# Kernel tuning notes

Hardware: AMD Instinct MI355X
Metric: run time of the kernel (lower is better)

Reference implementation:

```python
import jax, jax.numpy as jnp
import numpy as np

B, N, F = 4, 4096, 32
NG = 14  # number of gate graph-convs in GCNLSTM_Cell with memory state


def setup_inputs() -> dict:
    key = jax.random.key(0)
    ks = jax.random.split(key, 7)
    x = jax.random.normal(ks[0], (B, N, F), jnp.float32)
    h = jax.random.normal(ks[1], (B, N, F), jnp.float32)
    c = jax.random.normal(ks[2], (B, N, F), jnp.float32)
    m = jax.random.normal(ks[3], (B, N, F), jnp.float32)
    # weighted dense adjacency, scaled so row sums are O(1)
    adj = jax.random.uniform(ks[4], (N, N), jnp.float32) / N
    # 14 WeightedGraphConv layers: Dense F -> 2F (single FeedForward layer, no relu)
    W = jax.random.normal(ks[5], (NG, F, 2 * F), jnp.float32) * (1.0 / np.sqrt(F))
    b = jnp.zeros((NG, 2 * F), jnp.float32)
    return {"x": x, "h": h, "c": c, "m": m, "adj": adj, "W": W, "b": b}


def _gcn(ax, W, b):
    # ax: [B,N,F] = adj @ state (precomputed); Dense to 2F then GLU split.
    z = ax @ W + b  # [B,N,2F]
    ls, rs = jnp.split(z, 2, axis=-1)
    return ls * jax.nn.sigmoid(rs)


def reference(x, h, c, m, adj, W, b):
    # shared graph aggregation for x and h (adj is the same for all gates)
    ax = jnp.einsum('nm,bmf->bnf', adj, x)  # [B,N,F]
    ah = jnp.einsum('nm,bmf->bnf', adj, h)

    fx = _gcn(ax, W[0], b[0]); fh = _gcn(ah, W[1], b[1])
    ix = _gcn(ax, W[2], b[2]); ih = _gcn(ah, W[3], b[3])
    cx = _gcn(ax, W[4], b[4]); ch = _gcn(ah, W[5], b[5])
    ox = _gcn(ax, W[6], b[6]); oh = _gcn(ah, W[7], b[7])

    f = jax.nn.sigmoid(fx + fh)
    i = jax.nn.sigmoid(ix + ih)
    o = jax.nn.sigmoid(ox + oh)
    c_new = f * c + i * jnp.tanh(cx + ch)
    h1 = o * jnp.tanh(c_new)

    # memory-state block (6 more graph convs on h1 and m)
    ah1 = jnp.einsum('nm,bmf->bnf', adj, h1)
    am = jnp.einsum('nm,bmf->bnf', adj, m)
    sa_ih = _gcn(ah1, W[8], b[8]);  sa_im = _gcn(am, W[9], b[9])
    sa_gh = _gcn(ah1, W[10], b[10]); sa_gm = _gcn(am, W[11], b[11])
    sa_oh = _gcn(ah1, W[12], b[12]); sa_om = _gcn(am, W[13], b[13])

    i2 = jax.nn.sigmoid(sa_ih + sa_im)
    g = jax.nn.sigmoid(sa_gh + sa_gm)
    o2 = jax.nn.sigmoid(sa_oh + sa_om)
    m_new = i2 * m + (1.0 - i2) * g
    h_new = m_new * o2
    return h_new, c_new, m_new
```

## Files before the change

### kernel.cpp

```cpp
#include <hip/hip_runtime.h>
#include <stdint.h>

typedef __attribute__((ext_vector_type(4))) float f32x4;
typedef __attribute__((ext_vector_type(8))) short s16x8;

#define BB 4
#define NN 4096
#define FF 32
#define BNF (BB*NN*FF)

typedef __attribute__((address_space(3))) void       as3_void;
typedef const __attribute__((address_space(1))) void as1_cvoid;

#define WAITV4() asm volatile("s_waitcnt vmcnt(4)" ::: "memory")
#define WAITV0() asm volatile("s_waitcnt vmcnt(0)" ::: "memory")

static __device__ __forceinline__ float bf2f(uint16_t u) {
    union { uint32_t i; float f; } v; v.i = ((uint32_t)u) << 16; return v.f;
}
static __device__ __forceinline__ uint16_t f2bf(float f) {
    union { float f; uint32_t i; } v; v.f = f;
    uint32_t r = v.i + 0x7FFFu + ((v.i >> 16) & 1u);
    return (uint16_t)(r >> 16);
}
static __device__ __forceinline__ float sig_acc(float x) { return 1.0f / (1.0f + expf(-x)); }

static __device__ __forceinline__ void issue_tile_f(
    const float* __restrict__ base,
    float* sb, int w, int lane, int b, int n0)
{
    #pragma unroll
    for (int q = 0; q < 4; q++) {
        int r = w * 16 + q * 4 + (lane >> 4);
        int crow = (r < 32) ? (r + b * 32) : (r + 96 + b * 32);
        const float* gp = base + (size_t)crow * 4096 + n0 + (lane & 15) * 4;
        __builtin_amdgcn_global_load_lds((as1_cvoid*)gp,
            (as3_void*)(sb + (w * 16 + q * 4) * 64 + lane * 4), 16, 0, 0);
    }
}

__global__ __launch_bounds__(256) void prep_kernel(
    const float* __restrict__ adj, uint16_t* __restrict__ adjb, int cvtN,
    const float* __restrict__ Wf, uint16_t* __restrict__ Wp,
    const float* __restrict__ x, const float* __restrict__ h,
    const float* __restrict__ m,
    uint16_t* __restrict__ P, uint16_t* __restrict__ P2)
{
    int bid = blockIdx.x;
    int t = threadIdx.x;

    if (bid < cvtN) {
        size_t i = ((size_t)bid * 256 + t) * 8;
        float4 v0 = *(const float4*)(adj + i);
        float4 v1 = *(const float4*)(adj + i + 4);
        union { uint4 u; uint16_t e[8]; } o;
        o.e[0] = f2bf(v0.x); o.e[1] = f2bf(v0.y); o.e[2] = f2bf(v0.z); o.e[3] = f2bf(v0.w);
        o.e[4] = f2bf(v1.x); o.e[5] = f2bf(v1.y); o.e[6] = f2bf(v1.z); o.e[7] = f2bf(v1.w);
        *(uint4*)(adjb + i) = o.u;
        return;
    }
    bid -= cvtN;

    if (bid < 112) {
        int idx = bid * 256 + t;
        int g   = idx >> 11;
        int k   = (idx >> 6) & 31;
        int col = idx & 63;
        uint16_t v = f2bf(Wf[idx]);
        int gp = g >> 1;
        int sl = ((g & 1) << 2) | (k >> 3);
        int ph = sl ^ (col & 7);
        Wp[((gp * 64 + col) * 64) + ph * 8 + (k & 7)] = v;
        return;
    }
    bid -= 112;

    const float* src; uint16_t* dst; int rowbase, b, n0;
    if (bid < 512) {
        int tensor = bid >> 8;
        src = tensor ? h : x; dst = P; rowbase = tensor * 128;
        b = (bid >> 6) & 3; n0 = (bid & 63) * 64;
    } else {
        int q = bid - 512;
        src = m; dst = P2; rowbase = 128;
        b = q >> 6; n0 = (q & 63) * 64;
    }
    __shared__ uint16_t tl[32][65];
    {
        int i = t >> 2, ch = t & 3;
        size_t idx = ((size_t)(b * NN + n0 + i)) * FF + ch * 8;
        float4 v0 = *(const float4*)(src + idx);
        float4 v1 = *(const float4*)(src + idx + 4);
        uint16_t e[8] = { f2bf(v0.x), f2bf(v0.y), f2bf(v0.z), f2bf(v0.w),
                          f2bf(v1.x), f2bf(v1.y), f2bf(v1.z), f2bf(v1.w) };
        #pragma unroll
        for (int k = 0; k < 8; k++) tl[ch * 8 + k][i] = e[k];
    }
    __syncthreads();
    {
        int f = t >> 3, ch = t & 7;
        union { uint4 u; uint16_t e[8]; } v;
        #pragma unroll
        for (int k = 0; k < 8; k++) v.e[k] = tl[f][ch * 8 + k];
        size_t row = (size_t)(rowbase + b * 32 + f);
        *(uint4*)(dst + row * NN + n0 + ch * 8) = v.u;
    }
}

__global__ __launch_bounds__(256) void gemm_kernel(
    const void* __restrict__ Av,
    const uint16_t* __restrict__ Bt,
    float* __restrict__ part, uint16_t* __restrict__ Cb,
    int kLen, int direct, int isf32A)
{
    int mt = blockIdx.x, nt = blockIdx.y, ks = blockIdx.z;
    int m0 = mt * 128, c0 = nt * 128, k0 = ks * kLen;
    __shared__ __align__(16) uint16_t aL[128 * 32];
    __shared__ __align__(16) uint16_t bL[128 * 32];
    int t = threadIdx.x;
    int lane = t & 63, w = t >> 6;
    int wm = (w & 1) * 64, wn = (w >> 1) * 64;
    int lm = lane & 15, lk = lane >> 4;

    const uint16_t* A16 = (const uint16_t*)Av;
    const float*    Af  = (const float*)Av;

    f32x4 acc[4][4] = {};

    for (int kk = k0; kk < k0 + kLen; kk += 32) {
        if (!isf32A) {
            #pragma unroll
            for (int q = 0; q < 2; q++) {
                int pos  = q * 4096 + t * 16;
                int row  = pos >> 6;
                int slot = ((pos >> 4) & 3) ^ ((row >> 1) & 3);
                int col  = slot * 8;
                size_t aidx = (size_t)(m0 + row) * 4096 + kk + col;
                size_t bidx = (size_t)(c0 + row) * 4096 + kk + col;
                __builtin_amdgcn_global_load_lds((as1_cvoid*)(A16 + aidx),
                                                 (as3_void*)((char*)aL + pos), 16, 0, 0);
                __builtin_amdgcn_global_load_lds((as1_cvoid*)(Bt + bidx),
                                                 (as3_void*)((char*)bL + pos), 16, 0, 0);
            }
        } else {
            union { uint4 u; uint16_t e[8]; } sa[2], sb[2];
            #pragma unroll
            for (int q = 0; q < 2; q++) {
                int pos  = q * 4096 + t * 16;
                int row  = pos >> 6;
                int slot = ((pos >> 4) & 3) ^ ((row >> 1) & 3);
                int col  = slot * 8;
                size_t aidx = (size_t)(m0 + row) * 4096 + kk + col;
                size_t bidx = (size_t)(c0 + row) * 4096 + kk + col;
                union { uint4 u[2]; float f[8]; } va;
                va.u[0] = *(const uint4*)(Af + aidx);
                va.u[1] = *(const uint4*)(Af + aidx + 4);
                #pragma unroll
                for (int k = 0; k < 8; k++) sa[q].e[k] = f2bf(va.f[k]);
                sb[q].u = *(const uint4*)(Bt + bidx);
            }
            #pragma unroll
            for (int q = 0; q < 2; q++) {
                int pos = q * 4096 + t * 16;
                *(uint4*)((char*)aL + pos) = sa[q].u;
                *(uint4*)((char*)bL + pos) = sb[q].u;
            }
        }
        __syncthreads();
        s16x8 af[4], bfr[4];
        #pragma unroll
        for (int i = 0; i < 4; i++) {
            int r = wm + i * 16 + lm;
            af[i] = *(const s16x8*)(aL + r * 32 + ((lk ^ ((r >> 1) & 3)) * 8));
        }
        #pragma unroll
        for (int j = 0; j < 4; j++) {
            int r = wn + j * 16 + lm;
            bfr[j] = *(const s16x8*)(bL + r * 32 + ((lk ^ ((r >> 1) & 3)) * 8));
        }
        #pragma unroll
        for (int i = 0; i < 4; i++)
            #pragma unroll
            for (int j = 0; j < 4; j++)
                acc[i][j] = __builtin_amdgcn_mfma_f32_16x16x32_bf16(af[i], bfr[j], acc[i][j], 0, 0, 0);
        __syncthreads();
    }

    int r4 = (lane >> 4) * 4;
    if (direct) {
        #pragma unroll
        for (int i = 0; i < 4; i++)
            #pragma unroll
            for (int j = 0; j < 4; j++) {
                int c = c0 + wn + j * 16 + lm;
                int mr = m0 + wm + i * 16 + r4;
                union { uint2 u; uint16_t e[4]; } v;
                #pragma unroll
                for (int r = 0; r < 4; r++) v.e[r] = f2bf(acc[i][j][r]);
                *(uint2*)(Cb + (size_t)c * 4096 + mr) = v.u;
            }
    } else {
        #pragma unroll
        for (int i = 0; i < 4; i++)
            #pragma unroll
            for (int j = 0; j < 4; j++) {
                int c = c0 + wn + j * 16 + lm;
                int mr = m0 + wm + i * 16 + r4;
                *(f32x4*)(part + ((size_t)ks * 256 + c) * 4096 + mr) = acc[i][j];
            }
    }
}

__global__ __launch_bounds__(256) void fuse1_kernel(
    const float* __restrict__ part,
    const uint16_t* __restrict__ Cbi,
    const uint16_t* __restrict__ Wp,
    const float* __restrict__ bf_,
    const float* __restrict__ cf,
    float* __restrict__ cnew, uint16_t* __restrict__ S2t, int ns)
{
    __shared__ __align__(16) uint16_t WL[4 * 64 * 64];
    __shared__ __align__(16) float    AL[64 * 68];
    __shared__ __align__(16) float    BL[512];
    __shared__ __align__(16) uint16_t H1[32 * 72];
    __shared__ __align__(16) float    SB[2][64 * 64];

    int t = threadIdx.x;
    int lane = t & 63, w = t >> 6;
    int b = blockIdx.x >> 6, n0 = (blockIdx.x & 63) * 64;

    if (t < 128) *(float4*)(BL + t * 4) = *(const float4*)(bf_ + t * 4);

    #pragma unroll
    for (int q = 0; q < 8; q++) {
        int off = (w * 8 + q) * 512 + lane * 8;
        __builtin_amdgcn_global_load_lds((as1_cvoid*)(Wp + off),
                                         (as3_void*)(WL + off), 16, 0, 0);
    }

    int j = lane & 15, kg = lane >> 4;
    int r4 = kg * 4;

    float cv[2][4];
    #pragma unroll
    for (int hh = 0; hh < 2; hh++)
        #pragma unroll
        for (int r = 0; r < 4; r++)
            cv[hh][r] = cf[((size_t)(b * NN + n0 + w * 16 + r4 + r)) * FF + j + hh * 16];

    if (ns) {
        issue_tile_f(part, SB[0], w, lane, b, n0);
        if (ns > 1) issue_tile_f(part + (size_t)(256 * 4096), SB[1], w, lane, b, n0);
        float asum[16];
        #pragma unroll
        for (int i = 0; i < 16; i++) asum[i] = 0.0f;
        for (int ks = 0; ks < ns; ks++) {
            if (ks + 1 < ns) WAITV4(); else WAITV0();
            const float* sb = SB[ks & 1];
            #pragma unroll
            for (int i = 0; i < 16; i++)
                asum[i] += sb[(w * 16 + i) * 64 + lane];
            if (ks + 2 < ns)
                issue_tile_f(part + (size_t)(ks + 2) * (256 * 4096), SB[ks & 1], w, lane, b, n0);
        }
        #pragma unroll
        for (int i = 0; i < 16; i++) AL[(w * 16 + i) * 68 + lane] = asum[i];
    } else {
        int r = t >> 2, ch = t & 3;
        size_t crow = (r < 32) ? (size_t)(b * 32 + r) : (size_t)(128 + b * 32 + (r - 32));
        const uint16_t* cp = Cbi + crow * 4096 + n0 + ch * 16;
        union { uint4 u; uint16_t e[8]; } v0, v1;
        v0.u = *(const uint4*)(cp);
        v1.u = *(const uint4*)(cp + 8);
        float* al = AL + r * 68 + ch * 16;
        #pragma unroll
        for (int k = 0; k < 4; k++) {
            al[k]      = bf2f(v0.e[k]);  al[4 + k]  = bf2f(v0.e[4 + k]);
            al[8 + k]  = bf2f(v1.e[k]);  al[12 + k] = bf2f(v1.e[4 + k]);
        }
    }
    __syncthreads();

    s16x8 a_ax, a_ah;
    {
        int col = w * 16 + j;
        #pragma unroll
        for (int e = 0; e < 8; e++) {
            int k = kg * 8 + e;
            a_ax[e] = (short)f2bf(AL[k * 68 + col]);
            a_ah[e] = (short)f2bf(AL[(32 + k) * 68 + col]);
        }
    }

    float s[4][2][4];
    #pragma unroll
    for (int p = 0; p < 4; p++) {
        int g0 = p * 2, g1 = p * 2 + 1;
        f32x4 ac0[4] = {}, ac1[4] = {};
        #pragma unroll
        for (int ct = 0; ct < 4; ct++) {
            int col = ct * 16 + j;
            int ph0 = (kg)     ^ (col & 7);
            int ph1 = (4 + kg) ^ (col & 7);
            s16x8 b0 = *(const s16x8*)(WL + (p * 64 + col) * 64 + ph0 * 8);
            s16x8 b1 = *(const s16x8*)(WL + (p * 64 + col) * 64 + ph1 * 8);
            ac0[ct] = __builtin_amdgcn_mfma_f32_16x16x32_bf16(a_ax, b0, ac0[ct], 0, 0, 0);
            ac1[ct] = __builtin_amdgcn_mfma_f32_16x16x32_bf16(a_ah, b1, ac1[ct], 0, 0, 0);
        }
        #pragma unroll
        for (int hh = 0; hh < 2; hh++)
            #pragma unroll
            for (int r = 0; r < 4; r++) {
                float z0l = ac0[hh][r]     + BL[g0 * 64 + hh * 16 + j];
                float z0r = ac0[2 + hh][r] + BL[g0 * 64 + 32 + hh * 16 + j];
                float z1l = ac1[hh][r]     + BL[g1 * 64 + hh * 16 + j];
                float z1r = ac1[2 + hh][r] + BL[g1 * 64 + 32 + hh * 16 + j];
                s[p][hh][r] = z0l * sig_acc(z0r) + z1l * sig_acc(z1r);
            }
    }

    #pragma unroll
    for (int hh = 0; hh < 2; hh++) {
        union { uint2 u; uint16_t e[4]; } pk;
        #pragma unroll
        for (int r = 0; r < 4; r++) {
            size_t gidx = ((size_t)(b * NN + n0 + w * 16 + r4 + r)) * FF + j + hh * 16;
            float fg = sig_acc(s[0][hh][r]);
            float ig = sig_acc(s[1][hh][r]);
            float cc = tanhf(s[2][hh][r]);
            float og = sig_acc(s[3][hh][r]);
            float cn = fg * cv[hh][r] + ig * cc;
            cnew[gidx] = cn;
            pk.e[r] = f2bf(og * tanhf(cn));
        }
        *(uint2*)(H1 + (j + hh * 16) * 72 + w * 16 + r4) = pk.u;
    }
    __syncthreads();
    {
        int fr = t >> 3, ch = t & 7;
        uint4 v = *(const uint4*)(H1 + fr * 72 + ch * 8);
        *(uint4*)(S2t + ((size_t)(b * 32 + fr)) * NN + n0 + ch * 8) = v;
    }
}

__global__ __launch_bounds__(256) void fuse2_kernel(
    const float* __restrict__ part,
    const uint16_t* __restrict__ Cbi,
    const uint16_t* __restrict__ Wp,
    const float* __restrict__ bf_,
    const float* __restrict__ mf,
    float* __restrict__ hnew, float* __restrict__ mnew, int ns)
{
    __shared__ __align__(16) uint16_t WL[3 * 64 * 64];
    __shared__ __align__(16) float    AL[64 * 68];
    __shared__ __align__(16) float    BL[384];
    __shared__ __align__(16) float    SB[2][64 * 64];

    int t = threadIdx.x;
    int lane = t & 63, w = t >> 6;
    int b = blockIdx.x >> 6, n0 = (blockIdx.x & 63) * 64;

    if (t < 96) *(float4*)(BL + t * 4) = *(const float4*)(bf_ + 512 + t * 4);

    #pragma unroll
    for (int q = 0; q < 6; q++) {
        int off = (w * 6 + q) * 512 + lane * 8;
        __builtin_amdgcn_global_load_lds((as1_cvoid*)(Wp + 4 * 64 * 64 + off),
                                         (as3_void*)(WL + off), 16, 0, 0);
    }

    int j = lane & 15, kg = lane >> 4;
    int r4 = kg * 4;

    float mv[2][4];
    #pragma unroll
    for (int hh = 0; hh < 2; hh++)
        #pragma unroll
        for (int r = 0; r < 4; r++)
            mv[hh][r] = mf[((size_t)(b * NN + n0 + w * 16 + r4 + r)) * FF + j + hh * 16];

    if (ns) {
        issue_tile_f(part, SB[0], w, lane, b, n0);
        if (ns > 1) issue_tile_f(part + (size_t)(256 * 4096), SB[1], w, lane, b, n0);
        float asum[16];
        #pragma unroll
        for (int i = 0; i < 16; i++) asum[i] = 0.0f;
        for (int ks = 0; ks < ns; ks++) {
            if (ks + 1 < ns) WAITV4(); else WAITV0();
            const float* sb = SB[ks & 1];
            #pragma unroll
            for (int i = 0; i < 16; i++)
                asum[i] += sb[(w * 16 + i) * 64 + lane];
            if (ks + 2 < ns)
                issue_tile_f(part + (size_t)(ks + 2) * (256 * 4096), SB[ks & 1], w, lane, b, n0);
        }
        #pragma unroll
        for (int i = 0; i < 16; i++) AL[(w * 16 + i) * 68 + lane] = asum[i];
    } else {
        int r = t >> 2, ch = t & 3;
        size_t crow = (r < 32) ? (size_t)(b * 32 + r) : (size_t)(128 + b * 32 + (r - 32));
        const uint16_t* cp = Cbi + crow * 4096 + n0 + ch * 16;
        union { uint4 u; uint16_t e[8]; } v0, v1;
        v0.u = *(const uint4*)(cp);
        v1.u = *(const uint4*)(cp + 8);
        float* al = AL + r * 68 + ch * 16;
        #pragma unroll
        for (int k = 0; k < 4; k++) {
            al[k]      = bf2f(v0.e[k]);  al[4 + k]  = bf2f(v0.e[4 + k]);
            al[8 + k]  = bf2f(v1.e[k]);  al[12 + k] = bf2f(v1.e[4 + k]);
        }
    }
    __syncthreads();

    s16x8 a_h1, a_m;
    {
        int col = w * 16 + j;
        #pragma unroll
        for (int e = 0; e < 8; e++) {
            int k = kg * 8 + e;
            a_h1[e] = (short)f2bf(AL[k * 68 + col]);
            a_m[e]  = (short)f2bf(AL[(32 + k) * 68 + col]);
        }
    }

    float s[3][2][4];
    #pragma unroll
    for (int p = 0; p < 3; p++) {
        int g0 = p * 2, g1 = p * 2 + 1;
        f32x4 ac0[4] = {}, ac1[4] = {};
        #pragma unroll
        for (int ct = 0; ct < 4; ct++) {
            int col = ct * 16 + j;
            int ph0 = (kg)     ^ (col & 7);
            int ph1 = (4 + kg) ^ (col & 7);
            s16x8 b0 = *(const s16x8*)(WL + (p * 64 + col) * 64 + ph0 * 8);
            s16x8 b1 = *(const s16x8*)(WL + (p * 64 + col) * 64 + ph1 * 8);
            ac0[ct] = __builtin_amdgcn_mfma_f32_16x16x32_bf16(a_h1, b0, ac0[ct], 0, 0, 0);
            ac1[ct] = __builtin_amdgcn_mfma_f32_16x16x32_bf16(a_m, b1, ac1[ct], 0, 0, 0);
        }
        #pragma unroll
        for (int hh = 0; hh < 2; hh++)
            #pragma unroll
            for (int r = 0; r < 4; r++) {
                float z0l = ac0[hh][r]     + BL[g0 * 64 + hh * 16 + j];
                float z0r = ac0[2 + hh][r] + BL[g0 * 64 + 32 + hh * 16 + j];
                float z1l = ac1[hh][r]     + BL[g1 * 64 + hh * 16 + j];
                float z1r = ac1[2 + hh][r] + BL[g1 * 64 + 32 + hh * 16 + j];
                s[p][hh][r] = z0l * sig_acc(z0r) + z1l * sig_acc(z1r);
            }
    }

    #pragma unroll
    for (int hh = 0; hh < 2; hh++)
        #pragma unroll
        for (int r = 0; r < 4; r++) {
            size_t gidx = ((size_t)(b * NN + n0 + w * 16 + r4 + r)) * FF + j + hh * 16;
            float i2 = sig_acc(s[0][hh][r]);
            float gg = sig_acc(s[1][hh][r]);
            float o2 = sig_acc(s[2][hh][r]);
            float mn = i2 * mv[hh][r] + (1.0f - i2) * gg;
            mnew[gidx] = mn;
            hnew[gidx] = mn * o2;
        }
}

extern "C" void kernel_launch(void* const* d_in, const int* in_sizes, int n_in,
                              void* d_out, int out_size, void* d_ws, size_t ws_size,
                              hipStream_t stream) {
    (void)in_sizes; (void)n_in; (void)out_size;
    const float* x   = (const float*)d_in[0];
    const float* h   = (const float*)d_in[1];
    const float* c   = (const float*)d_in[2];
    const float* m   = (const float*)d_in[3];
    const float* adj = (const float*)d_in[4];
    const float* W   = (const float*)d_in[5];
    const float* bb  = (const float*)d_in[6];
    float* out = (float*)d_out;

    char* ws = (char*)d_ws;
    int haveAdjb = ws_size >= (size_t)(72u << 20);
    uint16_t* adjb = (uint16_t*)ws;
    size_t pOff = haveAdjb ? (size_t)(32u << 20) : 0;
    uint16_t* P    = (uint16_t*)(ws + pOff);
    uint16_t* P2   = (uint16_t*)(ws + pOff + (2u << 20));
    uint16_t* Cbuf = (uint16_t*)(ws + pOff + (4u << 20));
    uint16_t* Wp   = (uint16_t*)(ws + pOff + (6u << 20));
    size_t partOff = pOff + (7u << 20);
    float* part = (float*)(ws + partOff);

    if (ws_size < (8u << 20)) return;
    size_t avail = ws_size - partOff;
    int ns = 0;
    if      (avail >= (size_t)(32u << 20)) ns = 8;
    else if (avail >= (size_t)(16u << 20)) ns = 4;
    else if (avail >= (size_t)( 8u << 20)) ns = 2;
    else if (avail >= (size_t)( 4u << 20)) ns = 1;

    const void* Agemm = haveAdjb ? (const void*)adjb : (const void*)adj;
    int isf32A = haveAdjb ? 0 : 1;
    int cvtN = haveAdjb ? 8192 : 0;

    prep_kernel<<<cvtN + 112 + 768, 256, 0, stream>>>(adj, adjb, cvtN, W, Wp, x, h, m, P, P2);

    if (ns) {
        gemm_kernel<<<dim3(32, 2, ns), 256, 0, stream>>>(Agemm, P, part, nullptr, 4096 / ns, 0, isf32A);
    } else {
        gemm_kernel<<<dim3(32, 2, 1), 256, 0, stream>>>(Agemm, P, nullptr, Cbuf, 4096, 1, isf32A);
    }
    fuse1_kernel<<<256, 256, 0, stream>>>(part, Cbuf, Wp, bb, c, out + BNF, P2, ns);
    if (ns) {
        gemm_kernel<<<dim3(32, 2, ns), 256, 0, stream>>>(Agemm, P2, part, nullptr, 4096 / ns, 0, isf32A);
    } else {
        gemm_kernel<<<dim3(32, 2, 1), 256, 0, stream>>>(Agemm, P2, nullptr, Cbuf, 4096, 1, isf32A);
    }
    fuse2_kernel<<<256, 256, 0, stream>>>(part, Cbuf, Wp, bb, m, out, out + 2 * BNF, ns);
}
```

Before: 179.6 us.

## Split fuse kernels into single-wave blocks with direct global weight reads

The two fused epilogue kernels now launch 1024 single-wavefront blocks over 16-node tiles instead of 256 four-wave blocks over 64-node tiles. Split-K partials are summed in registers with simple one-ahead prefetch rather than async LDS double buffering. Weights and biases are read straight from global memory instead of being staged in LDS. The aim is more parallelism and less per-block LDS setup in these small kernels. In exchange, each block re-fetches the weights from global/L2 and loses the asynchronous LDS pipeline.

New measurement: 194.6 us. +8.3%, slower.

```diff
diff --git a/kernel.cpp b/kernel.cpp
--- a/kernel.cpp
+++ b/kernel.cpp
@@ -12,9 +12,6 @@
 typedef __attribute__((address_space(3))) void       as3_void;
 typedef const __attribute__((address_space(1))) void as1_cvoid;
 
-#define WAITV4() asm volatile("s_waitcnt vmcnt(4)" ::: "memory")
-#define WAITV0() asm volatile("s_waitcnt vmcnt(0)" ::: "memory")
-
 static __device__ __forceinline__ float bf2f(uint16_t u) {
     union { uint32_t i; float f; } v; v.i = ((uint32_t)u) << 16; return v.f;
 }
@@ -24,20 +21,6 @@
     return (uint16_t)(r >> 16);
 }
 static __device__ __forceinline__ float sig_acc(float x) { return 1.0f / (1.0f + expf(-x)); }
-
-static __device__ __forceinline__ void issue_tile_f(
-    const float* __restrict__ base,
-    float* sb, int w, int lane, int b, int n0)
-{
-    #pragma unroll
-    for (int q = 0; q < 4; q++) {
-        int r = w * 16 + q * 4 + (lane >> 4);
-        int crow = (r < 32) ? (r + b * 32) : (r + 96 + b * 32);
-        const float* gp = base + (size_t)crow * 4096 + n0 + (lane & 15) * 4;
-        __builtin_amdgcn_global_load_lds((as1_cvoid*)gp,
-            (as3_void*)(sb + (w * 16 + q * 4) * 64 + lane * 4), 16, 0, 0);
-    }
-}
 
 __global__ __launch_bounds__(256) void prep_kernel(
     const float* __restrict__ adj, uint16_t* __restrict__ adjb, int cvtN,
@@ -211,7 +194,7 @@
     }
 }
 
-__global__ __launch_bounds__(256) void fuse1_kernel(
+__global__ __launch_bounds__(64) void fuse1_kernel(
     const float* __restrict__ part,
     const uint16_t* __restrict__ Cbi,
     const uint16_t* __restrict__ Wp,
@@ -219,77 +202,68 @@
     const float* __restrict__ cf,
     float* __restrict__ cnew, uint16_t* __restrict__ S2t, int ns)
 {
-    __shared__ __align__(16) uint16_t WL[4 * 64 * 64];
-    __shared__ __align__(16) float    AL[64 * 68];
-    __shared__ __align__(16) float    BL[512];
-    __shared__ __align__(16) uint16_t H1[32 * 72];
-    __shared__ __align__(16) float    SB[2][64 * 64];
-
-    int t = threadIdx.x;
-    int lane = t & 63, w = t >> 6;
-    int b = blockIdx.x >> 6, n0 = (blockIdx.x & 63) * 64;
-
-    if (t < 128) *(float4*)(BL + t * 4) = *(const float4*)(bf_ + t * 4);
-
-    #pragma unroll
-    for (int q = 0; q < 8; q++) {
-        int off = (w * 8 + q) * 512 + lane * 8;
-        __builtin_amdgcn_global_load_lds((as1_cvoid*)(Wp + off),
-                                         (as3_void*)(WL + off), 16, 0, 0);
-    }
-
-    int j = lane & 15, kg = lane >> 4;
-    int r4 = kg * 4;
+    __shared__ float    AL[64 * 17];
+    __shared__ uint16_t H1[32 * 18];
+
+    int l = threadIdx.x;
+    int bid = blockIdx.x;
+    int b = bid >> 8, n0 = (bid & 255) * 16;
+    int j = l & 15, kg = l >> 4, r4 = kg * 4;
 
     float cv[2][4];
     #pragma unroll
     for (int hh = 0; hh < 2; hh++)
         #pragma unroll
         for (int r = 0; r < 4; r++)
-            cv[hh][r] = cf[((size_t)(b * NN + n0 + w * 16 + r4 + r)) * FF + j + hh * 16];
+            cv[hh][r] = cf[((size_t)(b * NN + n0 + r4 + r)) * FF + j + hh * 16];
+
+    int crow = (l < 32) ? (b * 32 + l) : (128 + b * 32 + (l - 32));
 
     if (ns) {
-        issue_tile_f(part, SB[0], w, lane, b, n0);
-        if (ns > 1) issue_tile_f(part + (size_t)(256 * 4096), SB[1], w, lane, b, n0);
-        float asum[16];
-        #pragma unroll
-        for (int i = 0; i < 16; i++) asum[i] = 0.0f;
+        const float* gp = part + (size_t)crow * 4096 + n0;
+        f32x4 c0 = *(const f32x4*)(gp);
+        f32x4 c1 = *(const f32x4*)(gp + 4);
+        f32x4 c2 = *(const f32x4*)(gp + 8);
+        f32x4 c3 = *(const f32x4*)(gp + 12);
+        f32x4 s0 = {}, s1 = {}, s2 = {}, s3 = {};
         for (int ks = 0; ks < ns; ks++) {
-            if (ks + 1 < ns) WAITV4(); else WAITV0();
-            const float* sb = SB[ks & 1];
-            #pragma unroll
-            for (int i = 0; i < 16; i++)
-                asum[i] += sb[(w * 16 + i) * 64 + lane];
-            if (ks + 2 < ns)
-                issue_tile_f(part + (size_t)(ks + 2) * (256 * 4096), SB[ks & 1], w, lane, b, n0);
-        }
-        #pragma unroll
-        for (int i = 0; i < 16; i++) AL[(w * 16 + i) * 68 + lane] = asum[i];
-    } else {
-        int r = t >> 2, ch = t & 3;
-        size_t crow = (r < 32) ? (size_t)(b * 32 + r) : (size_t)(128 + b * 32 + (r - 32));
-        const uint16_t* cp = Cbi + crow * 4096 + n0 + ch * 16;
+            f32x4 nv0, nv1, nv2, nv3;
+            if (ks + 1 < ns) {
+                const float* np = gp + (size_t)(ks + 1) * (256 * 4096);
+                nv0 = *(const f32x4*)(np);
+                nv1 = *(const f32x4*)(np + 4);
+                nv2 = *(const f32x4*)(np + 8);
+                nv3 = *(const f32x4*)(np + 12);
+            }
+            s0 += c0; s1 += c1; s2 += c2; s3 += c3;
+            if (ks + 1 < ns) { c0 = nv0; c1 = nv1; c2 = nv2; c3 = nv3; }
+        }
+        #pragma unroll
+        for (int e = 0; e < 4; e++) {
+            AL[l * 17 + e]      = s0[e];
+            AL[l * 17 + 4 + e]  = s1[e];
+            AL[l * 17 + 8 + e]  = s2[e];
+            AL[l * 17 + 12 + e] = s3[e];
+        }
+    } else {
+        const uint16_t* cp = Cbi + (size_t)crow * 4096 + n0;
         union { uint4 u; uint16_t e[8]; } v0, v1;
         v0.u = *(const uint4*)(cp);
         v1.u = *(const uint4*)(cp + 8);
-        float* al = AL + r * 68 + ch * 16;
-        #pragma unroll
-        for (int k = 0; k < 4; k++) {
-            al[k]      = bf2f(v0.e[k]);  al[4 + k]  = bf2f(v0.e[4 + k]);
-            al[8 + k]  = bf2f(v1.e[k]);  al[12 + k] = bf2f(v1.e[4 + k]);
+        #pragma unroll
+        for (int k = 0; k < 8; k++) {
+            AL[l * 17 + k]     = bf2f(v0.e[k]);
+            AL[l * 17 + 8 + k] = bf2f(v1.e[k]);
         }
     }
     __syncthreads();
 
     s16x8 a_ax, a_ah;
-    {
-        int col = w * 16 + j;
-        #pragma unroll
-        for (int e = 0; e < 8; e++) {
-            int k = kg * 8 + e;
-            a_ax[e] = (short)f2bf(AL[k * 68 + col]);
-            a_ah[e] = (short)f2bf(AL[(32 + k) * 68 + col]);
-        }
+    #pragma unroll
+    for (int e = 0; e < 8; e++) {
+        int k = kg * 8 + e;
+        a_ax[e] = (short)f2bf(AL[k * 17 + j]);
+        a_ah[e] = (short)f2bf(AL[(32 + k) * 17 + j]);
     }
 
     float s[4][2][4];
@@ -302,8 +276,8 @@
             int col = ct * 16 + j;
             int ph0 = (kg)     ^ (col & 7);
             int ph1 = (4 + kg) ^ (col & 7);
-            s16x8 b0 = *(const s16x8*)(WL + (p * 64 + col) * 64 + ph0 * 8);
-            s16x8 b1 = *(const s16x8*)(WL + (p * 64 + col) * 64 + ph1 * 8);
+            s16x8 b0 = *(const s16x8*)(Wp + (p * 64 + col) * 64 + ph0 * 8);
+            s16x8 b1 = *(const s16x8*)(Wp + (p * 64 + col) * 64 + ph1 * 8);
             ac0[ct] = __builtin_amdgcn_mfma_f32_16x16x32_bf16(a_ax, b0, ac0[ct], 0, 0, 0);
             ac1[ct] = __builtin_amdgcn_mfma_f32_16x16x32_bf16(a_ah, b1, ac1[ct], 0, 0, 0);
         }
@@ -311,39 +285,38 @@
         for (int hh = 0; hh < 2; hh++)
             #pragma unroll
             for (int r = 0; r < 4; r++) {
-                float z0l = ac0[hh][r]     + BL[g0 * 64 + hh * 16 + j];
-                float z0r = ac0[2 + hh][r] + BL[g0 * 64 + 32 + hh * 16 + j];
-                float z1l = ac1[hh][r]     + BL[g1 * 64 + hh * 16 + j];
-                float z1r = ac1[2 + hh][r] + BL[g1 * 64 + 32 + hh * 16 + j];
+                float z0l = ac0[hh][r]     + bf_[g0 * 64 + hh * 16 + j];
+                float z0r = ac0[2 + hh][r] + bf_[g0 * 64 + 32 + hh * 16 + j];
+                float z1l = ac1[hh][r]     + bf_[g1 * 64 + hh * 16 + j];
+                float z1r = ac1[2 + hh][r] + bf_[g1 * 64 + 32 + hh * 16 + j];
                 s[p][hh][r] = z0l * sig_acc(z0r) + z1l * sig_acc(z1r);
             }
     }
 
     #pragma unroll
-    for (int hh = 0; hh < 2; hh++) {
-        union { uint2 u; uint16_t e[4]; } pk;
+    for (int hh = 0; hh < 2; hh++)
         #pragma unroll
         for (int r = 0; r < 4; r++) {
-            size_t gidx = ((size_t)(b * NN + n0 + w * 16 + r4 + r)) * FF + j + hh * 16;
+            size_t gidx = ((size_t)(b * NN + n0 + r4 + r)) * FF + j + hh * 16;
             float fg = sig_acc(s[0][hh][r]);
             float ig = sig_acc(s[1][hh][r]);
             float cc = tanhf(s[2][hh][r]);
             float og = sig_acc(s[3][hh][r]);
             float cn = fg * cv[hh][r] + ig * cc;
             cnew[gidx] = cn;
-            pk.e[r] = f2bf(og * tanhf(cn));
-        }
-        *(uint2*)(H1 + (j + hh * 16) * 72 + w * 16 + r4) = pk.u;
-    }
+            H1[(j + hh * 16) * 18 + r4 + r] = f2bf(og * tanhf(cn));
+        }
     __syncthreads();
     {
-        int fr = t >> 3, ch = t & 7;
-        uint4 v = *(const uint4*)(H1 + fr * 72 + ch * 8);
-        *(uint4*)(S2t + ((size_t)(b * 32 + fr)) * NN + n0 + ch * 8) = v;
-    }
-}
-
-__global__ __launch_bounds__(256) void fuse2_kernel(
+        int f = l >> 1, half = l & 1;
+        union { uint4 u; uint16_t e[8]; } v;
+        #pragma unroll
+        for (int k = 0; k < 8; k++) v.e[k] = H1[f * 18 + half * 8 + k];
+        *(uint4*)(S2t + ((size_t)(b * 32 + f)) * NN + n0 + half * 8) = v.u;
+    }
+}
+
+__global__ __launch_bounds__(64) void fuse2_kernel(
     const float* __restrict__ part,
     const uint16_t* __restrict__ Cbi,
     const uint16_t* __restrict__ Wp,
@@ -351,77 +324,71 @@
     const float* __restrict__ mf,
     float* __restrict__ hnew, float* __restrict__ mnew, int ns)
 {
-    __shared__ __align__(16) uint16_t WL[3 * 64 * 64];
-    __shared__ __align__(16) float    AL[64 * 68];
-    __shared__ __align__(16) float    BL[384];
-    __shared__ __align__(16) float    SB[2][64 * 64];
-
-    int t = threadIdx.x;
-    int lane = t & 63, w = t >> 6;
-    int b = blockIdx.x >> 6, n0 = (blockIdx.x & 63) * 64;
-
-    if (t < 96) *(float4*)(BL + t * 4) = *(const float4*)(bf_ + 512 + t * 4);
-
-    #pragma unroll
-    for (int q = 0; q < 6; q++) {
-        int off = (w * 6 + q) * 512 + lane * 8;
-        __builtin_amdgcn_global_load_lds((as1_cvoid*)(Wp + 4 * 64 * 64 + off),
-                                         (as3_void*)(WL + off), 16, 0, 0);
-    }
-
-    int j = lane & 15, kg = lane >> 4;
-    int r4 = kg * 4;
+    __shared__ float AL[64 * 17];
+
+    int l = threadIdx.x;
+    int bid = blockIdx.x;
+    int b = bid >> 8, n0 = (bid & 255) * 16;
+    int j = l & 15, kg = l >> 4, r4 = kg * 4;
 
     float mv[2][4];
     #pragma unroll
     for (int hh = 0; hh < 2; hh++)
         #pragma unroll
         for (int r = 0; r < 4; r++)
-            mv[hh][r] = mf[((size_t)(b * NN + n0 + w * 16 + r4 + r)) * FF + j + hh * 16];
+            mv[hh][r] = mf[((size_t)(b * NN + n0 + r4 + r)) * FF + j + hh * 16];
+
+    int crow = (l < 32) ? (b * 32 + l) : (128 + b * 32 + (l - 32));
 
     if (ns) {
-        issue_tile_f(part, SB[0], w, lane, b, n0);
-        if (ns > 1) issue_tile_f(part + (size_t)(256 * 4096), SB[1], w, lane, b, n0);
-        float asum[16];
-        #pragma unroll
-        for (int i = 0; i < 16; i++) asum[i] = 0.0f;
+        const float* gp = part + (size_t)crow * 4096 + n0;
+        f32x4 c0 = *(const f32x4*)(gp);
+        f32x4 c1 = *(const f32x4*)(gp + 4);
+        f32x4 c2 = *(const f32x4*)(gp + 8);
+        f32x4 c3 = *(const f32x4*)(gp + 12);
+        f32x4 s0 = {}, s1 = {}, s2 = {}, s3 = {};
         for (int ks = 0; ks < ns; ks++) {
-            if (ks + 1 < ns) WAITV4(); else WAITV0();
-            const float* sb = SB[ks & 1];
-            #pragma unroll
-            for (int i = 0; i < 16; i++)
-                asum[i] += sb[(w * 16 + i) * 64 + lane];
-            if (ks + 2 < ns)
-                issue_tile_f(part + (size_t)(ks + 2) * (256 * 4096), SB[ks & 1], w, lane, b, n0);
-        }
-        #pragma unroll
-        for (int i = 0; i < 16; i++) AL[(w * 16 + i) * 68 + lane] = asum[i];
-    } else {
-        int r = t >> 2, ch = t & 3;
-        size_t crow = (r < 32) ? (size_t)(b * 32 + r) : (size_t)(128 + b * 32 + (r - 32));
-        const uint16_t* cp = Cbi + crow * 4096 + n0 + ch * 16;
+            f32x4 nv0, nv1, nv2, nv3;
+            if (ks + 1 < ns) {
+                const float* np = gp + (size_t)(ks + 1) * (256 * 4096);
+                nv0 = *(const f32x4*)(np);
+                nv1 = *(const f32x4*)(np + 4);
+                nv2 = *(const f32x4*)(np + 8);
+                nv3 = *(const f32x4*)(np + 12);
+            }
+            s0 += c0; s1 += c1; s2 += c2; s3 += c3;
+            if (ks + 1 < ns) { c0 = nv0; c1 = nv1; c2 = nv2; c3 = nv3; }
+        }
+        #pragma unroll
+        for (int e = 0; e < 4; e++) {
+            AL[l * 17 + e]      = s0[e];
+            AL[l * 17 + 4 + e]  = s1[e];
+            AL[l * 17 + 8 + e]  = s2[e];
+            AL[l * 17 + 12 + e] = s3[e];
+        }
+    } else {
+        const uint16_t* cp = Cbi + (size_t)crow * 4096 + n0;
         union { uint4 u; uint16_t e[8]; } v0, v1;
         v0.u = *(const uint4*)(cp);
         v1.u = *(const uint4*)(cp + 8);
-        float* al = AL + r * 68 + ch * 16;
-        #pragma unroll
-        for (int k = 0; k < 4; k++) {
-            al[k]      = bf2f(v0.e[k]);  al[4 + k]  = bf2f(v0.e[4 + k]);
-            al[8 + k]  = bf2f(v1.e[k]);  al[12 + k] = bf2f(v1.e[4 + k]);
+        #pragma unroll
+        for (int k = 0; k < 8; k++) {
+            AL[l * 17 + k]     = bf2f(v0.e[k]);
+            AL[l * 17 + 8 + k] = bf2f(v1.e[k]);
         }
     }
     __syncthreads();
 
     s16x8 a_h1, a_m;
-    {
-        int col = w * 16 + j;
-        #pragma unroll
-        for (int e = 0; e < 8; e++) {
-            int k = kg * 8 + e;
-            a_h1[e] = (short)f2bf(AL[k * 68 + col]);
-            a_m[e]  = (short)f2bf(AL[(32 + k) * 68 + col]);
-        }
-    }
+    #pragma unroll
+    for (int e = 0; e < 8; e++) {
+        int k = kg * 8 + e;
+        a_h1[e] = (short)f2bf(AL[k * 17 + j]);
+        a_m[e]  = (short)f2bf(AL[(32 + k) * 17 + j]);
+    }
+
+    const uint16_t* WpG = Wp + 4 * 64 * 64;
+    const float*    bG  = bf_ + 512;
 
     float s[3][2][4];
     #pragma unroll
@@ -433,8 +400,8 @@
             int col = ct * 16 + j;
             int ph0 = (kg)     ^ (col & 7);
             int ph1 = (4 + kg) ^ (col & 7);
-            s16x8 b0 = *(const s16x8*)(WL + (p * 64 + col) * 64 + ph0 * 8);
-            s16x8 b1 = *(const s16x8*)(WL + (p * 64 + col) * 64 + ph1 * 8);
+            s16x8 b0 = *(const s16x8*)(WpG + (p * 64 + col) * 64 + ph0 * 8);
+            s16x8 b1 = *(const s16x8*)(WpG + (p * 64 + col) * 64 + ph1 * 8);
             ac0[ct] = __builtin_amdgcn_mfma_f32_16x16x32_bf16(a_h1, b0, ac0[ct], 0, 0, 0);
             ac1[ct] = __builtin_amdgcn_mfma_f32_16x16x32_bf16(a_m, b1, ac1[ct], 0, 0, 0);
         }
@@ -442,10 +409,10 @@
         for (int hh = 0; hh < 2; hh++)
             #pragma unroll
             for (int r = 0; r < 4; r++) {
-                float z0l = ac0[hh][r]     + BL[g0 * 64 + hh * 16 + j];
-                float z0r = ac0[2 + hh][r] + BL[g0 * 64 + 32 + hh * 16 + j];
-                float z1l = ac1[hh][r]     + BL[g1 * 64 + hh * 16 + j];
-                float z1r = ac1[2 + hh][r] + BL[g1 * 64 + 32 + hh * 16 + j];
+                float z0l = ac0[hh][r]     + bG[g0 * 64 + hh * 16 + j];
+                float z0r = ac0[2 + hh][r] + bG[g0 * 64 + 32 + hh * 16 + j];
+                float z1l = ac1[hh][r]     + bG[g1 * 64 + hh * 16 + j];
+                float z1r = ac1[2 + hh][r] + bG[g1 * 64 + 32 + hh * 16 + j];
                 s[p][hh][r] = z0l * sig_acc(z0r) + z1l * sig_acc(z1r);
             }
     }
@@ -454,7 +421,7 @@
     for (int hh = 0; hh < 2; hh++)
         #pragma unroll
         for (int r = 0; r < 4; r++) {
-            size_t gidx = ((size_t)(b * NN + n0 + w * 16 + r4 + r)) * FF + j + hh * 16;
+            size_t gidx = ((size_t)(b * NN + n0 + r4 + r)) * FF + j + hh * 16;
             float i2 = sig_acc(s[0][hh][r]);
             float gg = sig_acc(s[1][hh][r]);
             float o2 = sig_acc(s[2][hh][r]);
@@ -507,11 +474,11 @@
     } else {
         gemm_kernel<<<dim3(32, 2, 1), 256, 0, stream>>>(Agemm, P, nullptr, Cbuf, 4096, 1, isf32A);
     }
-    fuse1_kernel<<<256, 256, 0, stream>>>(part, Cbuf, Wp, bb, c, out + BNF, P2, ns);
+    fuse1_kernel<<<1024, 64, 0, stream>>>(part, Cbuf, Wp, bb, c, out + BNF, P2, ns);
     if (ns) {
         gemm_kernel<<<dim3(32, 2, ns), 256, 0, stream>>>(Agemm, P2, part, nullptr, 4096 / ns, 0, isf32A);
     } else {
         gemm_kernel<<<dim3(32, 2, 1), 256, 0, stream>>>(Agemm, P2, nullptr, Cbuf, 4096, 1, isf32A);
     }
-    fuse2_kernel<<<256, 256, 0, stream>>>(part, Cbuf, Wp, bb, m, out, out + 2 * BNF, ns);
-}
+    fuse2_kernel<<<1024, 64, 0, stream>>>(part, Cbuf, Wp, bb, m, out, out + 2 * BNF, ns);
+}
```
